# Kernel optimization log

Measured on AMD Instinct MI355X. Metric: run time of the kernel, lower is better.

Reference implementation:

```python
import jax, jax.numpy as jnp
import numpy as np

DIMS = [3, 64, 64, 64, 3]  # [input_dim] + hidden dims + [input_dim]
TOTAL_W = sum(DIMS[l] * DIMS[l + 1] + 4 * DIMS[l + 1] for l in range(len(DIMS) - 1))  # 9356


def setup_inputs() -> dict:
    key = jax.random.key(0)
    k1, k2, k3 = jax.random.split(key, 3)
    B, N = 64, 8192
    context = jax.random.normal(k1, (B, N), dtype=jnp.float32)
    y = jax.random.normal(k2, (B, N, DIMS[0]), dtype=jnp.float32)
    tnw = jax.random.normal(k3, (B, TOTAL_W), dtype=jnp.float32) * 0.1
    return {"context": context, "y": y, "target_networks_weights": tnw}


def reference(context, y, target_networks_weights):
    B = target_networks_weights.shape[0]
    dx = y  # [B, N, dims[0]]
    i = 0
    n_layers = len(DIMS) - 1
    for l in range(n_layers):
        dl, dl1 = DIMS[l], DIMS[l + 1]
        W = target_networks_weights[:, i:i + dl * dl1].reshape(B, dl, dl1)
        i += dl * dl1
        bias = target_networks_weights[:, i:i + dl1]          # [B, dl1]
        i += dl1
        w_scale = target_networks_weights[:, i:i + dl1]        # [B, dl1]
        i += dl1
        b_scale = target_networks_weights[:, i:i + dl1]        # [B, dl1]
        i += dl1
        w_shift = target_networks_weights[:, i:i + dl1]        # [B, dl1]
        i += dl1
        # batched matmul + bias
        dx = jnp.einsum('bnd,bde->bne', dx, W) + bias[:, None, :]
        # sigmoid gate: bmm(context[:, :, None], w_scale[:, None, :]) = outer product
        scale = jax.nn.sigmoid(context[:, :, None] * w_scale[:, None, :] + b_scale[:, None, :])
        dx = scale * dx
        # shift term
        dx = dx + context[:, :, None] * w_shift[:, None, :]
        if l < n_layers - 1:
            dx = jax.nn.softplus(dx)
    return dx
```

## Files before the change

kernel.cpp:

```cpp
#include <hip/hip_runtime.h>
#include <math.h>

#define BB 64
#define NN 8192
#define TOTAL_W 9356

typedef _Float16 f16x8 __attribute__((ext_vector_type(8)));
typedef float f32x4 __attribute__((ext_vector_type(4)));
typedef float f32x2 __attribute__((ext_vector_type(2)));
typedef unsigned int u32x2 __attribute__((ext_vector_type(2)));

#define L2E 1.44269504088896340736f
#define LN2 0.6931471805599453f

#define WS_FILM 0
#define WS_A1   4096
#define WS_A2   12288
#define WS_A0   20480
#define WS_A3   24576
#define WSB     26624

#define FILM2_OFF 0
#define A1_OFF    4096
#define A2_OFF    12288
#define ACT_OFF   20480
#define LDS_BYTES (ACT_OFF + 128 * 128)

#define MFMA16(a, b, c) __builtin_amdgcn_mfma_f32_16x16x32_f16(a, b, c, 0, 0, 0)
#define EXP2 __builtin_amdgcn_exp2f
#define LOG2 __builtin_amdgcn_logf
#define RCPF __builtin_amdgcn_rcpf

__device__ __forceinline__ f32x2 pfma(f32x2 a, f32x2 b, f32x2 c) {
  return __builtin_elementwise_fma(a, b, c);
}

__device__ __forceinline__ const f32x4* film_base(const unsigned char* smem, int l, int qd) {
  return (const f32x4*)(smem + FILM2_OFF + ((l * 16 + qd) << 6));
}

template<bool SP>
__device__ __forceinline__ u32x2 film_quad(f32x4 acc, float ctx,
                                           f32x4 wscq, f32x4 bscq, f32x4 wshq) {
  f32x2 ctx2 = {ctx, ctx};
  f32x2 one = {1.f, 1.f};
  f32x2 z0 = pfma(ctx2, (f32x2){wscq.x, wscq.y}, (f32x2){bscq.x, bscq.y});
  f32x2 z1 = pfma(ctx2, (f32x2){wscq.z, wscq.w}, (f32x2){bscq.z, bscq.w});
  f32x2 d0 = {EXP2(-z0.x), EXP2(-z0.y)};  d0 += one;
  f32x2 d1 = {EXP2(-z1.x), EXP2(-z1.y)};  d1 += one;
  f32x2 s0 = {RCPF(d0.x), RCPF(d0.y)};
  f32x2 s1 = {RCPF(d1.x), RCPF(d1.y)};
  f32x2 v0 = pfma(ctx2, (f32x2){wshq.x, wshq.y}, s0 * (f32x2){acc.x, acc.y});
  f32x2 v1 = pfma(ctx2, (f32x2){wshq.z, wshq.w}, s1 * (f32x2){acc.z, acc.w});
  if (SP) {
    f32x2 l2 = {L2E, L2E}, ln = {LN2, LN2};
    f32x2 t0 = v0 * l2, t1 = v1 * l2;
    f32x2 u0 = {EXP2(t0.x), EXP2(t0.y)};  u0 += one;
    f32x2 u1 = {EXP2(t1.x), EXP2(t1.y)};  u1 += one;
    f32x2 g0 = {LOG2(u0.x), LOG2(u0.y)};
    f32x2 g1 = {LOG2(u1.x), LOG2(u1.y)};
    v0 = g0 * ln;
    v1 = g1 * ln;
  }
  auto p01 = __builtin_amdgcn_cvt_pkrtz(v0.x, v0.y);
  auto p23 = __builtin_amdgcn_cvt_pkrtz(v1.x, v1.y);
  u32x2 w;
  w.x = __builtin_bit_cast(unsigned int, p01);
  w.y = __builtin_bit_cast(unsigned int, p23);
  return w;
}

__device__ __forceinline__ void act_store(unsigned char* smem, int pt, int slot, u32x2 w) {
  int pos = ((((slot >> 1) ^ (pt & 7)) << 1) | (slot & 1));
  *(u32x2*)(smem + ACT_OFF + pt * 128 + (pos << 3)) = w;
}
__device__ __forceinline__ f16x8 act_load(const unsigned char* smem, int pt, int pair) {
  int gr = pair ^ (pt & 7);
  return *(const f16x8*)(smem + ACT_OFF + pt * 128 + (gr << 4));
}

__global__ __launch_bounds__(512)
void ode_prep_kernel(const float* __restrict__ tnw, unsigned char* __restrict__ ws) {
  const int b = blockIdx.x;
  const int tid = threadIdx.x;
  const float* __restrict__ wb = tnw + (size_t)b * TOTAL_W;
  unsigned char* __restrict__ wsb = ws + (size_t)b * WSB;

  if (tid < 64) {
    const int biaso[4] = {192, 4544, 8896, 9344};
    const int dim[4] = {64, 64, 64, 3};
#pragma unroll
    for (int l = 0; l < 4; ++l) {
      float bv = 0.f, wscv = 0.f, bscv = 0.f, wshv = 0.f;
      if (tid < dim[l]) {
        int bo = biaso[l], d = dim[l];
        bv = wb[bo + tid];
        wscv = wb[bo + d + tid] * L2E;
        bscv = wb[bo + 2 * d + tid] * L2E;
        wshv = wb[bo + 3 * d + tid];
      }
      float* f2 = (float*)(wsb + WS_FILM + ((l * 16 + (tid >> 2)) << 6)) + (tid & 3);
      f2[0] = bv;
      f2[4] = wscv;
      f2[8] = bscv;
      f2[12] = wshv;
    }
  }
#pragma unroll
  for (int L = 0; L < 2; ++L) {
    const int woff = L ? 4800 : 448;
    unsigned char* dst = wsb + (L ? WS_A2 : WS_A1);
    int r = tid;
    int lane_r = r & 63;
    int t = (r >> 6) & 1;
    int m = r >> 7;
    int f_out = 16 * m + (lane_r & 15);
    int f_in0 = 32 * t + 8 * (lane_r >> 4);
    f16x8 h;
#pragma unroll
    for (int i = 0; i < 8; ++i) h[i] = (_Float16)wb[woff + (f_in0 + i) * 64 + f_out];
    *(f16x8*)(dst + r * 16) = h;
  }
  if (tid < 256) {
    int m = tid >> 6;
    int lane = tid & 63;
    int g = lane >> 4, col = lane & 15;
    f16x8 h = {0, 0, 0, 0, 0, 0, 0, 0};
    if (g == 0) {
#pragma unroll
      for (int i = 0; i < 3; ++i) h[i] = (_Float16)wb[i * 64 + 16 * m + col];
    }
    *(f16x8*)(wsb + WS_A0 + tid * 16) = h;
  }
  if (tid < 128) {
    int t = tid >> 6;
    int lane = tid & 63;
    int g = lane >> 4, col = lane & 15;
    f16x8 h = {0, 0, 0, 0, 0, 0, 0, 0};
    if (col < 3) {
#pragma unroll
      for (int i = 0; i < 8; ++i)
        h[i] = (_Float16)wb[9152 + (32 * t + 8 * g + i) * 3 + col];
    }
    *(f16x8*)(wsb + WS_A3 + tid * 16) = h;
  }
}

__global__ __launch_bounds__(256)
void ode_hypernet_kernel(const float* __restrict__ context,
                         const float* __restrict__ y,
                         const unsigned char* __restrict__ ws,
                         float* __restrict__ out) {
  __shared__ __align__(16) unsigned char smem[LDS_BYTES];
  const int b = blockIdx.y;
  const int tid = threadIdx.x;
  const unsigned char* __restrict__ wsb = ws + (size_t)b * WSB;

  const int lane = tid & 63;
  const int wid = tid >> 6;
  const int g = lane >> 4;
  const int col = lane & 15;

#pragma unroll
  for (int it = 0; it < 5; ++it) {
    int i = tid + it * 256;
    *(f32x4*)(smem + i * 16) = *(const f32x4*)(wsb + i * 16);
  }
  f16x8 A0r[4];
#pragma unroll
  for (int m = 0; m < 4; ++m)
    A0r[m] = *(const f16x8*)(wsb + WS_A0 + (m * 64 + lane) * 16);
  f16x8 A3r0 = *(const f16x8*)(wsb + WS_A3 + lane * 16);
  f16x8 A3r1 = *(const f16x8*)(wsb + WS_A3 + (64 + lane) * 16);
  __syncthreads();

  const int pt0 = wid * 32 + col;
  const int pt1 = pt0 + 16;

  const int nb = blockIdx.x * 256;
  const size_t cb = (size_t)b * NN;
  float ctxs[4], yv[4][3];
#pragma unroll
  for (int k = 0; k < 4; ++k) {
    int n = nb + (k >> 1) * 128 + pt0 + (k & 1) * 16;
    ctxs[k] = context[cb + n];
    const float* yp = y + (cb + n) * 3;
    yv[k][0] = yp[0]; yv[k][1] = yp[1]; yv[k][2] = yp[2];
  }

#pragma unroll
  for (int ss = 0; ss < 2; ++ss) {
    const float ctx0 = ctxs[ss * 2], ctx1 = ctxs[ss * 2 + 1];
    const int n0 = nb + ss * 128 + pt0;
    const int n1 = n0 + 16;

    f16x8 By0 = {0, 0, 0, 0, 0, 0, 0, 0};
    f16x8 By1 = {0, 0, 0, 0, 0, 0, 0, 0};
    if (g == 0) {
      By0[0] = (_Float16)yv[ss * 2][0];
      By0[1] = (_Float16)yv[ss * 2][1];
      By0[2] = (_Float16)yv[ss * 2][2];
      By1[0] = (_Float16)yv[ss * 2 + 1][0];
      By1[1] = (_Float16)yv[ss * 2 + 1][1];
      By1[2] = (_Float16)yv[ss * 2 + 1][2];
    }

#pragma unroll
    for (int m = 0; m < 4; ++m) {
      const f32x4* fb = film_base(smem, 0, 4 * m + g);
      f32x4 biasq = fb[0], wscq = fb[1], bscq = fb[2], wshq = fb[3];
      f32x4 c0 = biasq, c1 = biasq;
      c0 = MFMA16(A0r[m], By0, c0);
      c1 = MFMA16(A0r[m], By1, c1);
      act_store(smem, pt0, 4 * m + g, film_quad<true>(c0, ctx0, wscq, bscq, wshq));
      act_store(smem, pt1, 4 * m + g, film_quad<true>(c1, ctx1, wscq, bscq, wshq));
    }

#pragma unroll
    for (int L = 1; L <= 2; ++L) {
      const int aoff = (L == 1) ? A1_OFF : A2_OFF;
      f16x8 B00 = act_load(smem, pt0, g);
      f16x8 B01 = act_load(smem, pt0, 4 + g);
      f16x8 B10 = act_load(smem, pt1, g);
      f16x8 B11 = act_load(smem, pt1, 4 + g);
#pragma unroll
      for (int m = 0; m < 4; ++m) {
        const f32x4* fb = film_base(smem, L, 4 * m + g);
        f32x4 biasq = fb[0], wscq = fb[1], bscq = fb[2], wshq = fb[3];
        f16x8 a0 = *(const f16x8*)(smem + aoff + ((m * 2 + 0) * 64 + lane) * 16);
        f16x8 a1 = *(const f16x8*)(smem + aoff + ((m * 2 + 1) * 64 + lane) * 16);
        f32x4 c0 = biasq, c1 = biasq;
        c0 = MFMA16(a0, B00, c0);
        c0 = MFMA16(a1, B01, c0);
        c1 = MFMA16(a0, B10, c1);
        c1 = MFMA16(a1, B11, c1);
        act_store(smem, pt0, 4 * m + g, film_quad<true>(c0, ctx0, wscq, bscq, wshq));
        act_store(smem, pt1, 4 * m + g, film_quad<true>(c1, ctx1, wscq, bscq, wshq));
      }
    }

    {
      f16x8 B00 = act_load(smem, pt0, g);
      f16x8 B01 = act_load(smem, pt0, 4 + g);
      f16x8 B10 = act_load(smem, pt1, g);
      f16x8 B11 = act_load(smem, pt1, 4 + g);
      const f32x4* fb = film_base(smem, 3, g);
      f32x4 biasq = fb[0], wscq = fb[1], bscq = fb[2], wshq = fb[3];
      f32x4 c0 = biasq, c1 = biasq;
      c0 = MFMA16(A3r0, B00, c0);
      c0 = MFMA16(A3r1, B01, c0);
      c1 = MFMA16(A3r0, B10, c1);
      c1 = MFMA16(A3r1, B11, c1);
      if (g == 0) {
#pragma unroll
        for (int p = 0; p < 2; ++p) {
          f32x4 c = p ? c1 : c0;
          float ctx = p ? ctx1 : ctx0;
          int n = p ? n1 : n0;
#pragma unroll
          for (int j = 0; j < 3; ++j) {
            float z = fmaf(ctx, wscq[j], bscq[j]);
            float s = RCPF(1.0f + EXP2(-z));
            float v = fmaf(ctx, wshq[j], s * c[j]);
            out[((size_t)b * NN + n) * 3 + j] = v;
          }
        }
      }
    }
  }
}

extern "C" void kernel_launch(void* const* d_in, const int* in_sizes, int n_in,
                              void* d_out, int out_size, void* d_ws, size_t ws_size,
                              hipStream_t stream) {
  const float* context = (const float*)d_in[0];
  const float* y       = (const float*)d_in[1];
  const float* tnw     = (const float*)d_in[2];
  float* out           = (float*)d_out;
  unsigned char* ws    = (unsigned char*)d_ws;

  ode_prep_kernel<<<dim3(BB, 1, 1), dim3(512, 1, 1), 0, stream>>>(tnw, ws);
  dim3 grid(NN / 256, BB, 1);
  dim3 block(256, 1, 1);
  ode_hypernet_kernel<<<grid, block, 0, stream>>>(context, y, ws, out);
}
```

Measured before the change: 55.46 us.

## Keep activations in registers using 16x16x16 MFMA layout instead of LDS round-trip

Switches from 16x16x32 MFMA to 16x16x16 MFMA so each layer's output accumulator fragment matches the B-operand fragment the next layer needs. Activations then stay in registers across layers instead of going through swizzled LDS stores and loads. The prep kernel repacks the weight tiles into 4-element fragments, and the LDS footprint shrinks. The trade-off is twice as many MFMA instructions, each with half the K depth, plus more VGPR pressure from holding the activation arrays.

Result: no change. 56.08 us (+1.1%).

```diff
diff --git a/kernel.cpp b/kernel.cpp
--- a/kernel.cpp
+++ b/kernel.cpp
@@ -5,7 +5,7 @@
 #define NN 8192
 #define TOTAL_W 9356
 
-typedef _Float16 f16x8 __attribute__((ext_vector_type(8)));
+typedef _Float16 f16x4 __attribute__((ext_vector_type(4)));
 typedef float f32x4 __attribute__((ext_vector_type(4)));
 typedef float f32x2 __attribute__((ext_vector_type(2)));
 typedef unsigned int u32x2 __attribute__((ext_vector_type(2)));
@@ -17,16 +17,19 @@
 #define WS_A1   4096
 #define WS_A2   12288
 #define WS_A0   20480
-#define WS_A3   24576
-#define WSB     26624
+#define WS_A3   22528
+#define WSB     24576
 
 #define FILM2_OFF 0
 #define A1_OFF    4096
 #define A2_OFF    12288
-#define ACT_OFF   20480
-#define LDS_BYTES (ACT_OFF + 128 * 128)
-
-#define MFMA16(a, b, c) __builtin_amdgcn_mfma_f32_16x16x32_f16(a, b, c, 0, 0, 0)
+#define LDS_BYTES 20480
+
+#if __has_builtin(__builtin_amdgcn_mfma_f32_16x16x16_f16)
+#define MFMAK16(a, b, c) __builtin_amdgcn_mfma_f32_16x16x16_f16(a, b, c, 0, 0, 0)
+#else
+#define MFMAK16(a, b, c) __builtin_amdgcn_mfma_f32_16x16x16f16(a, b, c, 0, 0, 0)
+#endif
 #define EXP2 __builtin_amdgcn_exp2f
 #define LOG2 __builtin_amdgcn_logf
 #define RCPF __builtin_amdgcn_rcpf
@@ -40,7 +43,7 @@
 }
 
 template<bool SP>
-__device__ __forceinline__ u32x2 film_quad(f32x4 acc, float ctx,
+__device__ __forceinline__ f16x4 film_quad(f32x4 acc, float ctx,
                                            f32x4 wscq, f32x4 bscq, f32x4 wshq) {
   f32x2 ctx2 = {ctx, ctx};
   f32x2 one = {1.f, 1.f};
@@ -67,16 +70,12 @@
   u32x2 w;
   w.x = __builtin_bit_cast(unsigned int, p01);
   w.y = __builtin_bit_cast(unsigned int, p23);
-  return w;
-}
-
-__device__ __forceinline__ void act_store(unsigned char* smem, int pt, int slot, u32x2 w) {
-  int pos = ((((slot >> 1) ^ (pt & 7)) << 1) | (slot & 1));
-  *(u32x2*)(smem + ACT_OFF + pt * 128 + (pos << 3)) = w;
-}
-__device__ __forceinline__ f16x8 act_load(const unsigned char* smem, int pt, int pair) {
-  int gr = pair ^ (pt & 7);
-  return *(const f16x8*)(smem + ACT_OFF + pt * 128 + (gr << 4));
+  return __builtin_bit_cast(f16x4, w);
+}
+
+__device__ __forceinline__ f16x4 a_tile(const unsigned char* smem, int aoff,
+                                        int m, int t, int lane) {
+  return *(const f16x4*)(smem + aoff + (((m * 4 + t) * 64 + lane) << 3));
 }
 
 __global__ __launch_bounds__(512)
@@ -110,39 +109,42 @@
   for (int L = 0; L < 2; ++L) {
     const int woff = L ? 4800 : 448;
     unsigned char* dst = wsb + (L ? WS_A2 : WS_A1);
-    int r = tid;
-    int lane_r = r & 63;
-    int t = (r >> 6) & 1;
-    int m = r >> 7;
-    int f_out = 16 * m + (lane_r & 15);
-    int f_in0 = 32 * t + 8 * (lane_r >> 4);
-    f16x8 h;
-#pragma unroll
-    for (int i = 0; i < 8; ++i) h[i] = (_Float16)wb[woff + (f_in0 + i) * 64 + f_out];
-    *(f16x8*)(dst + r * 16) = h;
+#pragma unroll
+    for (int it = 0; it < 2; ++it) {
+      int idx = tid + it * 512;
+      int lane = idx & 63;
+      int tile = idx >> 6;
+      int m = tile >> 2, t = tile & 3;
+      int f_out = 16 * m + (lane & 15);
+      int f_in0 = 16 * t + 4 * (lane >> 4);
+      f16x4 h;
+#pragma unroll
+      for (int i = 0; i < 4; ++i) h[i] = (_Float16)wb[woff + (f_in0 + i) * 64 + f_out];
+      *(f16x4*)(dst + idx * 8) = h;
+    }
   }
   if (tid < 256) {
     int m = tid >> 6;
     int lane = tid & 63;
-    int g = lane >> 4, col = lane & 15;
-    f16x8 h = {0, 0, 0, 0, 0, 0, 0, 0};
-    if (g == 0) {
-#pragma unroll
-      for (int i = 0; i < 3; ++i) h[i] = (_Float16)wb[i * 64 + 16 * m + col];
-    }
-    *(f16x8*)(wsb + WS_A0 + tid * 16) = h;
-  }
-  if (tid < 128) {
+    int kg = lane >> 4, row = lane & 15;
+    f16x4 h = {0, 0, 0, 0};
+    if (kg == 0) {
+#pragma unroll
+      for (int i = 0; i < 3; ++i) h[i] = (_Float16)wb[i * 64 + 16 * m + row];
+    }
+    *(f16x4*)(wsb + WS_A0 + tid * 8) = h;
+  }
+  if (tid < 256) {
     int t = tid >> 6;
     int lane = tid & 63;
-    int g = lane >> 4, col = lane & 15;
-    f16x8 h = {0, 0, 0, 0, 0, 0, 0, 0};
-    if (col < 3) {
-#pragma unroll
-      for (int i = 0; i < 8; ++i)
-        h[i] = (_Float16)wb[9152 + (32 * t + 8 * g + i) * 3 + col];
-    }
-    *(f16x8*)(wsb + WS_A3 + tid * 16) = h;
+    int kg = lane >> 4, row = lane & 15;
+    f16x4 h = {0, 0, 0, 0};
+    if (row < 3) {
+#pragma unroll
+      for (int i = 0; i < 4; ++i)
+        h[i] = (_Float16)wb[9152 + (16 * t + 4 * kg + i) * 3 + row];
+    }
+    *(f16x4*)(wsb + WS_A3 + tid * 8) = h;
   }
 }
 
@@ -166,19 +168,19 @@
     int i = tid + it * 256;
     *(f32x4*)(smem + i * 16) = *(const f32x4*)(wsb + i * 16);
   }
-  f16x8 A0r[4];
+  f16x4 A0r[4], A3r[4];
 #pragma unroll
   for (int m = 0; m < 4; ++m)
-    A0r[m] = *(const f16x8*)(wsb + WS_A0 + (m * 64 + lane) * 16);
-  f16x8 A3r0 = *(const f16x8*)(wsb + WS_A3 + lane * 16);
-  f16x8 A3r1 = *(const f16x8*)(wsb + WS_A3 + (64 + lane) * 16);
+    A0r[m] = *(const f16x4*)(wsb + WS_A0 + ((m * 64 + lane) << 3));
+#pragma unroll
+  for (int t = 0; t < 4; ++t)
+    A3r[t] = *(const f16x4*)(wsb + WS_A3 + ((t * 64 + lane) << 3));
   __syncthreads();
 
   const int pt0 = wid * 32 + col;
-  const int pt1 = pt0 + 16;
-
   const int nb = blockIdx.x * 256;
   const size_t cb = (size_t)b * NN;
+
   float ctxs[4], yv[4][3];
 #pragma unroll
   for (int k = 0; k < 4; ++k) {
@@ -194,8 +196,7 @@
     const int n0 = nb + ss * 128 + pt0;
     const int n1 = n0 + 16;
 
-    f16x8 By0 = {0, 0, 0, 0, 0, 0, 0, 0};
-    f16x8 By1 = {0, 0, 0, 0, 0, 0, 0, 0};
+    f16x4 By0 = {0, 0, 0, 0}, By1 = {0, 0, 0, 0};
     if (g == 0) {
       By0[0] = (_Float16)yv[ss * 2][0];
       By0[1] = (_Float16)yv[ss * 2][1];
@@ -205,52 +206,58 @@
       By1[2] = (_Float16)yv[ss * 2 + 1][2];
     }
 
+    f16x4 Bc0[4], Bc1[4], Bd0[4], Bd1[4];
+
 #pragma unroll
     for (int m = 0; m < 4; ++m) {
       const f32x4* fb = film_base(smem, 0, 4 * m + g);
       f32x4 biasq = fb[0], wscq = fb[1], bscq = fb[2], wshq = fb[3];
       f32x4 c0 = biasq, c1 = biasq;
-      c0 = MFMA16(A0r[m], By0, c0);
-      c1 = MFMA16(A0r[m], By1, c1);
-      act_store(smem, pt0, 4 * m + g, film_quad<true>(c0, ctx0, wscq, bscq, wshq));
-      act_store(smem, pt1, 4 * m + g, film_quad<true>(c1, ctx1, wscq, bscq, wshq));
-    }
-
-#pragma unroll
-    for (int L = 1; L <= 2; ++L) {
-      const int aoff = (L == 1) ? A1_OFF : A2_OFF;
-      f16x8 B00 = act_load(smem, pt0, g);
-      f16x8 B01 = act_load(smem, pt0, 4 + g);
-      f16x8 B10 = act_load(smem, pt1, g);
-      f16x8 B11 = act_load(smem, pt1, 4 + g);
-#pragma unroll
-      for (int m = 0; m < 4; ++m) {
-        const f32x4* fb = film_base(smem, L, 4 * m + g);
-        f32x4 biasq = fb[0], wscq = fb[1], bscq = fb[2], wshq = fb[3];
-        f16x8 a0 = *(const f16x8*)(smem + aoff + ((m * 2 + 0) * 64 + lane) * 16);
-        f16x8 a1 = *(const f16x8*)(smem + aoff + ((m * 2 + 1) * 64 + lane) * 16);
-        f32x4 c0 = biasq, c1 = biasq;
-        c0 = MFMA16(a0, B00, c0);
-        c0 = MFMA16(a1, B01, c0);
-        c1 = MFMA16(a0, B10, c1);
-        c1 = MFMA16(a1, B11, c1);
-        act_store(smem, pt0, 4 * m + g, film_quad<true>(c0, ctx0, wscq, bscq, wshq));
-        act_store(smem, pt1, 4 * m + g, film_quad<true>(c1, ctx1, wscq, bscq, wshq));
-      }
+      c0 = MFMAK16(A0r[m], By0, c0);
+      c1 = MFMAK16(A0r[m], By1, c1);
+      Bc0[m] = film_quad<true>(c0, ctx0, wscq, bscq, wshq);
+      Bc1[m] = film_quad<true>(c1, ctx1, wscq, bscq, wshq);
+    }
+
+#pragma unroll
+    for (int m = 0; m < 4; ++m) {
+      const f32x4* fb = film_base(smem, 1, 4 * m + g);
+      f32x4 biasq = fb[0], wscq = fb[1], bscq = fb[2], wshq = fb[3];
+      f32x4 c0 = biasq, c1 = biasq;
+#pragma unroll
+      for (int t = 0; t < 4; ++t) {
+        f16x4 a = a_tile(smem, A1_OFF, m, t, lane);
+        c0 = MFMAK16(a, Bc0[t], c0);
+        c1 = MFMAK16(a, Bc1[t], c1);
+      }
+      Bd0[m] = film_quad<true>(c0, ctx0, wscq, bscq, wshq);
+      Bd1[m] = film_quad<true>(c1, ctx1, wscq, bscq, wshq);
+    }
+
+#pragma unroll
+    for (int m = 0; m < 4; ++m) {
+      const f32x4* fb = film_base(smem, 2, 4 * m + g);
+      f32x4 biasq = fb[0], wscq = fb[1], bscq = fb[2], wshq = fb[3];
+      f32x4 c0 = biasq, c1 = biasq;
+#pragma unroll
+      for (int t = 0; t < 4; ++t) {
+        f16x4 a = a_tile(smem, A2_OFF, m, t, lane);
+        c0 = MFMAK16(a, Bd0[t], c0);
+        c1 = MFMAK16(a, Bd1[t], c1);
+      }
+      Bc0[m] = film_quad<true>(c0, ctx0, wscq, bscq, wshq);
+      Bc1[m] = film_quad<true>(c1, ctx1, wscq, bscq, wshq);
     }
 
     {
-      f16x8 B00 = act_load(smem, pt0, g);
-      f16x8 B01 = act_load(smem, pt0, 4 + g);
-      f16x8 B10 = act_load(smem, pt1, g);
-      f16x8 B11 = act_load(smem, pt1, 4 + g);
       const f32x4* fb = film_base(smem, 3, g);
       f32x4 biasq = fb[0], wscq = fb[1], bscq = fb[2], wshq = fb[3];
       f32x4 c0 = biasq, c1 = biasq;
-      c0 = MFMA16(A3r0, B00, c0);
-      c0 = MFMA16(A3r1, B01, c0);
-      c1 = MFMA16(A3r0, B10, c1);
-      c1 = MFMA16(A3r1, B11, c1);
+#pragma unroll
+      for (int t = 0; t < 4; ++t) {
+        c0 = MFMAK16(A3r[t], Bc0[t], c0);
+        c1 = MFMAK16(A3r[t], Bc1[t], c1);
+      }
       if (g == 0) {
 #pragma unroll
         for (int p = 0; p < 2; ++p) {
```
